# Kernel optimization log

Measured on AMD Instinct MI355X. Metric: run time of the kernel, lower is better.

Reference implementation:

```python
import jax, jax.numpy as jnp
import numpy as np
import math

N_HEAD = 16

def setup_inputs() -> dict:
    key = jax.random.key(0)
    ks = jax.random.split(key, 10)
    B, T, C = 4, 1024, 1024
    s = 0.02
    return {
        "x": jax.random.normal(ks[0], (B, T, C), jnp.float32),
        "visual_features": jax.random.normal(ks[1], (B, C), jnp.float32),
        "Wq": jax.random.normal(ks[2], (C, C), jnp.float32) * s,
        "bq": jax.random.normal(ks[3], (C,), jnp.float32) * s,
        "Wk": jax.random.normal(ks[4], (C, C), jnp.float32) * s,
        "bk": jax.random.normal(ks[5], (C,), jnp.float32) * s,
        "Wv": jax.random.normal(ks[6], (C, C), jnp.float32) * s,
        "bv": jax.random.normal(ks[7], (C,), jnp.float32) * s,
        "Wp": jax.random.normal(ks[8], (C, C), jnp.float32) * s,
        "bp": jax.random.normal(ks[9], (C,), jnp.float32) * s,
    }

def reference(x, visual_features, Wq, bq, Wk, bk, Wv, bv, Wp, bp):
    B, T, C = x.shape
    H = N_HEAD
    dh = C // H
    # visual_features is broadcast to every query position; project once
    # (identical math to projecting the expanded [B,T,C] tensor).
    q = (x @ Wq + bq).reshape(B, T, H, dh).transpose(0, 2, 1, 3)      # [B,H,T,dh]
    kv = visual_features @ Wk + bk                                     # [B,C]
    k = kv.reshape(B, 1, H, dh).transpose(0, 2, 1, 3)                  # [B,H,1,dh]
    vv = visual_features @ Wv + bv
    v = vv.reshape(B, 1, H, dh).transpose(0, 2, 1, 3)                  # [B,H,1,dh]
    k = jnp.broadcast_to(k, (B, H, T, dh))                             # keys identical over T
    v = jnp.broadcast_to(v, (B, H, T, dh))
    scale = 1.0 / math.sqrt(dh)
    att = jnp.einsum("bhqd,bhkd->bhqk", q, k) * scale                  # [B,H,T,T]
    att = jax.nn.softmax(att, axis=-1)
    y = jnp.einsum("bhqk,bhkd->bhqd", att, v)                          # [B,H,T,dh]
    y = y.transpose(0, 2, 1, 3).reshape(B, T, C)
    return y @ Wp + bp
```

## Files before the change

### kernel.cpp

```cpp
#include <hip/hip_runtime.h>

#define BB 4
#define TT 1024
#define CC 1024
#define SK 32
#define KC (CC / SK)
#define RPT 4

__global__ void __launch_bounds__(256)
fused_gemv(const float* __restrict__ vf,
           const float* __restrict__ Wv, const float* __restrict__ bv,
           const float* __restrict__ Wp, const float* __restrict__ bp,
           float* __restrict__ z)
{
    __shared__ float vfT[CC][BB];
    __shared__ float red[8][BB][KC];
    __shared__ float vvc[BB][KC];

    const int t  = threadIdx.x;
    const int jb = blockIdx.x;
    const int c  = blockIdx.y;
    const int i0 = c * KC;

#pragma unroll
    for (int r = 0; r < 4; ++r) {
        int k = t + r * 256;
        float4 vq;
        vq.x = vf[0 * CC + k];
        vq.y = vf[1 * CC + k];
        vq.z = vf[2 * CC + k];
        vq.w = vf[3 * CC + k];
        *reinterpret_cast<float4*>(&vfT[k][0]) = vq;
    }
    __syncthreads();

    {
        const int ii = t & (KC - 1);
        const int g  = t >> 5;
        const int i  = i0 + ii;
        float p0 = 0.f, p1 = 0.f, p2 = 0.f, p3 = 0.f;
#pragma unroll 8
        for (int kk = 0; kk < 128; ++kk) {
            int k = g * 128 + kk;
            float w  = Wv[k * CC + i];
            float4 vq = *reinterpret_cast<const float4*>(&vfT[k][0]);
            p0 += vq.x * w;
            p1 += vq.y * w;
            p2 += vq.z * w;
            p3 += vq.w * w;
        }
        red[g][0][ii] = p0;
        red[g][1][ii] = p1;
        red[g][2][ii] = p2;
        red[g][3][ii] = p3;
    }
    __syncthreads();
    if (t < BB * KC) {
        const int b = t >> 5, i2 = t & (KC - 1);
        float s = bv[i0 + i2];
#pragma unroll
        for (int gg = 0; gg < 8; ++gg) s += red[gg][b][i2];
        vvc[b][i2] = s;
    }
    __syncthreads();

    const int j = jb * 256 + t;
    float acc0 = bp[j] * (1.0f / SK);
    float acc1 = acc0, acc2 = acc0, acc3 = acc0;
#pragma unroll
    for (int q4 = 0; q4 < KC / 4; ++q4) {
        float4 v0 = *reinterpret_cast<const float4*>(&vvc[0][q4 * 4]);
        float4 v1 = *reinterpret_cast<const float4*>(&vvc[1][q4 * 4]);
        float4 v2 = *reinterpret_cast<const float4*>(&vvc[2][q4 * 4]);
        float4 v3 = *reinterpret_cast<const float4*>(&vvc[3][q4 * 4]);
        float w0 = Wp[(i0 + q4 * 4 + 0) * CC + j];
        float w1 = Wp[(i0 + q4 * 4 + 1) * CC + j];
        float w2 = Wp[(i0 + q4 * 4 + 2) * CC + j];
        float w3 = Wp[(i0 + q4 * 4 + 3) * CC + j];
        acc0 += v0.x * w0 + v0.y * w1 + v0.z * w2 + v0.w * w3;
        acc1 += v1.x * w0 + v1.y * w1 + v1.z * w2 + v1.w * w3;
        acc2 += v2.x * w0 + v2.y * w1 + v2.z * w2 + v2.w * w3;
        acc3 += v3.x * w0 + v3.y * w1 + v3.z * w2 + v3.w * w3;
    }
    atomicAdd(&z[0 * CC + j], acc0);
    atomicAdd(&z[1 * CC + j], acc1);
    atomicAdd(&z[2 * CC + j], acc2);
    atomicAdd(&z[3 * CC + j], acc3);
}

__global__ void __launch_bounds__(256)
bcast_rows(const float* __restrict__ z, float* __restrict__ out) {
    int tid  = blockIdx.x * blockDim.x + threadIdx.x;
    int idx4 = tid << 2;
    int c  = idx4 & (CC - 1);
    int bt = idx4 >> 10;
    int b  = bt >> 8;
    int t0 = (bt & 255) * RPT;
    float4 v = *reinterpret_cast<const float4*>(z + b * CC + c);
    float* dst = out + ((size_t)(b * TT + t0) << 10) + c;
#pragma unroll
    for (int r = 0; r < RPT; ++r) {
        *reinterpret_cast<float4*>(dst) = v;
        dst += CC;
    }
}

extern "C" void kernel_launch(void* const* d_in, const int* in_sizes, int n_in,
                              void* d_out, int out_size, void* d_ws, size_t ws_size,
                              hipStream_t stream) {
    const float* vf = (const float*)d_in[1];
    const float* Wv = (const float*)d_in[6];
    const float* bv = (const float*)d_in[7];
    const float* Wp = (const float*)d_in[8];
    const float* bp = (const float*)d_in[9];
    float* out = (float*)d_out;

    float* z = (float*)d_ws;

    fused_gemv<<<dim3(CC / 256, SK), 256, 0, stream>>>(vf, Wv, bv, Wp, bp, z);
    bcast_rows<<<(BB * TT * CC / 4 / RPT) / 256, 256, 0, stream>>>(z, out);
}
```

Baseline: 99.37 us.

## Split GEMV K-dimension finer and replicate atomic accumulation buffers

Raises the split-K factor of the fused value/projection GEMV from 32 to 128 chunks, so more blocks run in parallel and each block does less serial work. The Wv reduction is restructured to use 32 groups with interleaved rows. Atomic accumulation into z is spread across 4 replica buffers to reduce contention, and the broadcast kernel sums the replicas. This adds more redundant Wv reads per block and extra z reads in the broadcast kernel, and it assumes the workspace is zeroed and large enough for 4 replicas.

New measurement: 100.7 us. Within noise of the previous version (+1.3%).

```diff
diff --git a/kernel.cpp b/kernel.cpp
--- a/kernel.cpp
+++ b/kernel.cpp
@@ -3,8 +3,9 @@
 #define BB 4
 #define TT 1024
 #define CC 1024
-#define SK 32
-#define KC (CC / SK)
+#define SKZ 128
+#define KCZ (CC / SKZ)
+#define REP 4
 #define RPT 4
 
 __global__ void __launch_bounds__(256)
@@ -13,14 +14,14 @@
            const float* __restrict__ Wp, const float* __restrict__ bp,
            float* __restrict__ z)
 {
-    __shared__ float vfT[CC][BB];
-    __shared__ float red[8][BB][KC];
-    __shared__ float vvc[BB][KC];
+    __shared__ float4 vfT[CC];
+    __shared__ float  red[32][BB][KCZ + 1];
+    __shared__ float  vvc[BB][KCZ];
 
     const int t  = threadIdx.x;
     const int jb = blockIdx.x;
     const int c  = blockIdx.y;
-    const int i0 = c * KC;
+    const int i0 = c * KCZ;
 
 #pragma unroll
     for (int r = 0; r < 4; ++r) {
@@ -30,20 +31,20 @@
         vq.y = vf[1 * CC + k];
         vq.z = vf[2 * CC + k];
         vq.w = vf[3 * CC + k];
-        *reinterpret_cast<float4*>(&vfT[k][0]) = vq;
+        vfT[k] = vq;
     }
     __syncthreads();
 
     {
-        const int ii = t & (KC - 1);
-        const int g  = t >> 5;
+        const int ii = t & (KCZ - 1);
+        const int g  = t >> 3;
         const int i  = i0 + ii;
         float p0 = 0.f, p1 = 0.f, p2 = 0.f, p3 = 0.f;
-#pragma unroll 8
-        for (int kk = 0; kk < 128; ++kk) {
-            int k = g * 128 + kk;
+#pragma unroll
+        for (int kk = 0; kk < 32; ++kk) {
+            int k = kk * 32 + g;
             float w  = Wv[k * CC + i];
-            float4 vq = *reinterpret_cast<const float4*>(&vfT[k][0]);
+            float4 vq = vfT[k];
             p0 += vq.x * w;
             p1 += vq.y * w;
             p2 += vq.z * w;
@@ -55,37 +56,31 @@
         red[g][3][ii] = p3;
     }
     __syncthreads();
-    if (t < BB * KC) {
-        const int b = t >> 5, i2 = t & (KC - 1);
+    if (t < BB * KCZ) {
+        const int b = t >> 3, i2 = t & (KCZ - 1);
         float s = bv[i0 + i2];
 #pragma unroll
-        for (int gg = 0; gg < 8; ++gg) s += red[gg][b][i2];
+        for (int g = 0; g < 32; ++g) s += red[g][b][i2];
         vvc[b][i2] = s;
     }
     __syncthreads();
 
     const int j = jb * 256 + t;
-    float acc0 = bp[j] * (1.0f / SK);
+    float acc0 = bp[j] * (1.0f / SKZ);
     float acc1 = acc0, acc2 = acc0, acc3 = acc0;
 #pragma unroll
-    for (int q4 = 0; q4 < KC / 4; ++q4) {
-        float4 v0 = *reinterpret_cast<const float4*>(&vvc[0][q4 * 4]);
-        float4 v1 = *reinterpret_cast<const float4*>(&vvc[1][q4 * 4]);
-        float4 v2 = *reinterpret_cast<const float4*>(&vvc[2][q4 * 4]);
-        float4 v3 = *reinterpret_cast<const float4*>(&vvc[3][q4 * 4]);
-        float w0 = Wp[(i0 + q4 * 4 + 0) * CC + j];
-        float w1 = Wp[(i0 + q4 * 4 + 1) * CC + j];
-        float w2 = Wp[(i0 + q4 * 4 + 2) * CC + j];
-        float w3 = Wp[(i0 + q4 * 4 + 3) * CC + j];
-        acc0 += v0.x * w0 + v0.y * w1 + v0.z * w2 + v0.w * w3;
-        acc1 += v1.x * w0 + v1.y * w1 + v1.z * w2 + v1.w * w3;
-        acc2 += v2.x * w0 + v2.y * w1 + v2.z * w2 + v2.w * w3;
-        acc3 += v3.x * w0 + v3.y * w1 + v3.z * w2 + v3.w * w3;
+    for (int q = 0; q < KCZ; ++q) {
+        float w = Wp[(i0 + q) * CC + j];
+        acc0 += vvc[0][q] * w;
+        acc1 += vvc[1][q] * w;
+        acc2 += vvc[2][q] * w;
+        acc3 += vvc[3][q] * w;
     }
-    atomicAdd(&z[0 * CC + j], acc0);
-    atomicAdd(&z[1 * CC + j], acc1);
-    atomicAdd(&z[2 * CC + j], acc2);
-    atomicAdd(&z[3 * CC + j], acc3);
+    float* zr = z + (c & (REP - 1)) * (BB * CC);
+    atomicAdd(&zr[0 * CC + j], acc0);
+    atomicAdd(&zr[1 * CC + j], acc1);
+    atomicAdd(&zr[2 * CC + j], acc2);
+    atomicAdd(&zr[3 * CC + j], acc3);
 }
 
 __global__ void __launch_bounds__(256)
@@ -96,7 +91,16 @@
     int bt = idx4 >> 10;
     int b  = bt >> 8;
     int t0 = (bt & 255) * RPT;
-    float4 v = *reinterpret_cast<const float4*>(z + b * CC + c);
+    const float* zb = z + b * CC + c;
+    float4 v0 = *reinterpret_cast<const float4*>(zb + 0 * BB * CC);
+    float4 v1 = *reinterpret_cast<const float4*>(zb + 1 * BB * CC);
+    float4 v2 = *reinterpret_cast<const float4*>(zb + 2 * BB * CC);
+    float4 v3 = *reinterpret_cast<const float4*>(zb + 3 * BB * CC);
+    float4 v;
+    v.x = (v0.x + v1.x) + (v2.x + v3.x);
+    v.y = (v0.y + v1.y) + (v2.y + v3.y);
+    v.z = (v0.z + v1.z) + (v2.z + v3.z);
+    v.w = (v0.w + v1.w) + (v2.w + v3.w);
     float* dst = out + ((size_t)(b * TT + t0) << 10) + c;
 #pragma unroll
     for (int r = 0; r < RPT; ++r) {
@@ -117,6 +121,6 @@
 
     float* z = (float*)d_ws;
 
-    fused_gemv<<<dim3(CC / 256, SK), 256, 0, stream>>>(vf, Wv, bv, Wp, bp, z);
+    fused_gemv<<<dim3(CC / 256, SKZ), 256, 0, stream>>>(vf, Wv, bv, Wp, bp, z);
     bcast_rows<<<(BB * TT * CC / 4 / RPT) / 256, 256, 0, stream>>>(z, out);
 }
```
